# Kernel tuning notes

Measured on AMD Instinct MI355X. Metric: run time of the kernel, lower is better.

Reference implementation:

```python
import jax, jax.numpy as jnp
import numpy as np

K = 256       # num states
M = 2         # markov order
D = 256       # lemb_size
V = 50000     # ntypes (vocab)
T = 512
B = 256
Kp1 = K + 1
EPS = 1e-5
INIT = 0.1


def _layernorm(h, g, b):
    mu = h.mean(-1, keepdims=True)
    var = ((h - mu) ** 2).mean(-1, keepdims=True)
    return (h - mu) / jnp.sqrt(var + EPS) * g + b


def setup_inputs() -> dict:
    key = jax.random.key(0)
    ks = jax.random.split(key, 12)
    u = lambda k, shp: jax.random.uniform(k, shp, jnp.float32, -INIT, INIT)
    return {
        "x": jax.random.randint(ks[0], (T, B), 0, V, dtype=jnp.int32),
        "z": jax.random.randint(ks[1], (T, B), 0, K, dtype=jnp.int32),
        "lembs": u(ks[2], (K, D)),
        "tlembs": u(ks[3], (Kp1, D)),
        "dec_W": u(ks[4], (V, D)),
        "dec_b": jnp.zeros((V,), jnp.float32),
        "em_W": u(ks[5], (D, D)),
        "em_bias": jnp.zeros((D,), jnp.float32),
        "em_g": jnp.ones((D,), jnp.float32),
        "em_beta": jnp.zeros((D,), jnp.float32),
        "td_W": u(ks[6], (K, M * D)),
        "td_b": jnp.zeros((K,), jnp.float32),
        "tm_W": u(ks[7], (M * D, M * D)),
        "tm_bias": jnp.zeros((M * D,), jnp.float32),
        "tn_g": jnp.ones((M * D,), jnp.float32),
        "tn_beta": jnp.zeros((M * D,), jnp.float32),
    }


def reference(x, z, lembs, tlembs, dec_W, dec_b, em_W, em_bias, em_g, em_beta,
              td_W, td_b, tm_W, tm_bias, tn_g, tn_beta):
    # --- emission distribution: K x V log-normalized ---
    h = _layernorm(lembs + jax.nn.relu(lembs @ em_W.T + em_bias), em_g, em_beta)
    emdist = jax.nn.log_softmax(h @ dec_W.T + dec_b, axis=1)  # (K, V)

    # --- transition distribution: (Kp1^M, K) log-normalized ---
    # cartesian product of label embeddings, row-major: row r <-> (i_0,...,i_{M-1})
    idx = jnp.indices((Kp1,) * M).reshape(M, -1)                 # (M, Kp1^M)
    cat = tlembs[idx].transpose(1, 0, 2).reshape(-1, M * D)      # (Kp1^M, M*D)
    th = _layernorm(cat + jax.nn.relu(cat @ tm_W.T + tm_bias), tn_g, tn_beta)
    transdist = jax.nn.log_softmax(th @ td_W.T + td_b, axis=1)   # (Kp1^M, K)

    # --- log_joint ---
    xlps = emdist.T[x]                                           # (T, B, K)
    emlps = jnp.take_along_axis(xlps, z[..., None].astype(jnp.int32), axis=2)[..., 0].sum(0)  # (B,)

    zpad = jnp.concatenate([jnp.full((M, B), K, dtype=z.dtype), z], axis=0)  # (T+M, B)
    win = jnp.stack([zpad[m:m + T] for m in range(M + 1)], 0)    # (M+1, T, B)
    lin = win[0]
    for m in range(1, M):
        lin = lin * Kp1 + win[m]                                 # row index into (Kp1^M, K)
    trans_lps = transdist[lin, win[M]]                           # (T, B)
    return emlps + trans_lps.sum(0)                              # (B,)
```

## Files before the change

### kernel.cpp

```cpp
#include <hip/hip_runtime.h>

#define Kst 256
#define Dd 256
#define Vv 50000
#define VPAD 50176
#define Tt 512
#define Bb 256
#define KP1 257
#define MD 512
#define NROWS (KP1*KP1)
#define EPSf 1e-5f

#define VB2 196
#define VB3 (VB2*4)
#define EMB 800

typedef __attribute__((ext_vector_type(8))) short short8;
typedef __attribute__((ext_vector_type(4))) float f32x4;
typedef __attribute__((ext_vector_type(4))) unsigned u32x4;
typedef __attribute__((ext_vector_type(2))) unsigned u32x2;

__device__ __forceinline__ unsigned short f2bf(float f) {
    unsigned u = __builtin_bit_cast(unsigned, f);
    unsigned r = (u + 0x7fffu + ((u >> 16) & 1u)) >> 16;
    return (unsigned short)r;
}
__device__ __forceinline__ float bf2f(unsigned short u) {
    return __builtin_bit_cast(float, ((unsigned)u) << 16);
}
__device__ __forceinline__ unsigned bfpack(float lo, float hi) {
    return __builtin_amdgcn_perm(__builtin_bit_cast(unsigned, hi),
                                 __builtin_bit_cast(unsigned, lo), 0x07060302u);
}
__device__ __forceinline__ unsigned f2bf2(float lo, float hi) {
    return (unsigned)f2bf(lo) | ((unsigned)f2bf(hi) << 16);
}

__global__ __launch_bounds__(256) void k_hP(
    const float* __restrict__ lembs, const float* __restrict__ em_W,
    const float* __restrict__ em_bias, const float* __restrict__ em_g,
    const float* __restrict__ em_beta, unsigned short* __restrict__ h_bf,
    const float* __restrict__ tlembs, const float* __restrict__ tm_W,
    float* __restrict__ P0, float* __restrict__ P1,
    const float* __restrict__ td_W, const float* __restrict__ tn_g,
    const float* __restrict__ tn_beta, const float* __restrict__ td_b,
    unsigned short* __restrict__ tdwg_bf, float* __restrict__ Gt,
    float* __restrict__ Bt, const float* __restrict__ dec_W,
    unsigned short* __restrict__ dwP)
{
    int bid = blockIdx.x;
    int tid = threadIdx.x, lane = tid & 63, wv = tid >> 6;
    int l15 = lane & 15, q = lane >> 4;

    if (bid >= 108) {
        int pb = bid - 108;
        int vb2 = pb >> 1, sub = pb & 1;
        #pragma unroll 2
        for (int j = 0; j < 8; ++j) {
            int E0 = sub*4096 + wv*1024 + j*128 + lane*2;
            #pragma unroll
            for (int b = 0; b < 2; ++b) {
                int E = E0 + b;
                int ks = E >> 10, fi = (E >> 6) & 15, le = E & 63;
                int q2 = le >> 4, lv = le & 15;
                int v = ((fi >> 2) << 6) + lv*4 + (fi & 3);
                int row = vb2*256 + v;
                if (row > Vv-1) row = Vv-1;
                const float* src = dec_W + (size_t)row*Dd + ks*32 + q2*8;
                float4 f0 = *(const float4*)(src);
                float4 f1 = *(const float4*)(src + 4);
                u32x4 pk;
                pk.x = bfpack(f0.x, f0.y);
                pk.y = bfpack(f0.z, f0.w);
                pk.z = bfpack(f1.x, f1.y);
                pk.w = bfpack(f1.z, f1.w);
                *(short8*)(dwP + ((size_t)vb2*8192 + E)*8) = __builtin_bit_cast(short8, pk);
            }
        }
        return;
    }

    if (bid >= 44) {
        int c = (bid - 44)*4 + wv;
        const float4* w4 = (const float4*)(td_W + (size_t)c*MD);
        const float4* g4 = (const float4*)tn_g;
        const float4* b4 = (const float4*)tn_beta;
        float sg = 0.f, sb = 0.f;
        short8 o;
        #pragma unroll
        for (int u = 0; u < 2; ++u) {
            int j4 = lane*2 + u;
            float4 w = w4[j4], g = g4[j4], bt = b4[j4];
            sg += w.x*g.x + w.y*g.y + w.z*g.z + w.w*g.w;
            sb += w.x*bt.x + w.y*bt.y + w.z*bt.z + w.w*bt.w;
            o[u*4+0] = (short)f2bf(w.x*g.x);
            o[u*4+1] = (short)f2bf(w.y*g.y);
            o[u*4+2] = (short)f2bf(w.z*g.z);
            o[u*4+3] = (short)f2bf(w.w*g.w);
        }
        {
            int wvv = c >> 6, l15v = (c >> 2) & 15, ctv = c & 3;
            int ksv = lane >> 2, qv = lane & 3;
            *(short8*)(tdwg_bf +
                ((((size_t)wvv*16 + ksv)*4 + ctv)*64 + (qv*16 + l15v))*8) = o;
        }
        #pragma unroll
        for (int dd = 32; dd > 0; dd >>= 1) {
            sg += __shfl_xor(sg, dd);
            sb += __shfl_xor(sb, dd);
        }
        if (lane == 0) { Gt[c] = sg; Bt[c] = sb + td_b[c]; }
        return;
    }

    __shared__ short ta[32][264];
    __shared__ float lsep[4][32][2];
    __shared__ float musig[32][2];

    int job, r0, cb, koff, BK;
    const float* Arow; const float* Brow;
    if (bid < 8) {
        job = 0; r0 = bid*32; cb = 0; koff = 0; BK = Dd;
        Arow = lembs; Brow = em_W;
    } else {
        int b2 = bid - 8;
        int half = b2 / 18;
        int b3 = b2 % 18;
        job = 1 + half;
        r0 = (b3 >> 1) * 32;
        cb = (b3 & 1) * 256;
        koff = half * 256; BK = MD;
        Arow = tlembs; Brow = tm_W;
    }

    {
        int row = tid >> 3, seg = (tid & 7) * 32;
        int r = r0 + row;
        if (r > 256) r = 256;
        const float4* s4 = (const float4*)(Arow + (size_t)r*Dd + seg);
        #pragma unroll
        for (int u = 0; u < 4; ++u) {
            float4 f0 = s4[u*2], f1 = s4[u*2+1];
            u32x4 pk;
            pk.x = bfpack(f0.x, f0.y);
            pk.y = bfpack(f0.z, f0.w);
            pk.z = bfpack(f1.x, f1.y);
            pk.w = bfpack(f1.z, f1.w);
            *(short8*)&ta[row][seg + u*8] = __builtin_bit_cast(short8, pk);
        }
    }
    __syncthreads();

    const float* bptr[4];
    #pragma unroll
    for (int ct = 0; ct < 4; ++ct) {
        int j = cb + wv*64 + ct*16 + l15;
        bptr[ct] = Brow + (size_t)j*BK + koff + q*8;
    }
    f32x4 acc[2][4];
    #pragma unroll
    for (int rt = 0; rt < 2; ++rt)
        #pragma unroll
        for (int ct = 0; ct < 4; ++ct)
            acc[rt][ct] = (f32x4){0.f,0.f,0.f,0.f};
    for (int ks = 0; ks < 8; ++ks) {
        short8 a0 = *(const short8*)&ta[ 0 + l15][ks*32 + q*8];
        short8 a1 = *(const short8*)&ta[16 + l15][ks*32 + q*8];
        short8 b[4];
        #pragma unroll
        for (int ct = 0; ct < 4; ++ct) {
            float4 f0 = *(const float4*)(bptr[ct] + ks*32);
            float4 f1 = *(const float4*)(bptr[ct] + ks*32 + 4);
            u32x4 pk;
            pk.x = bfpack(f0.x, f0.y);
            pk.y = bfpack(f0.z, f0.w);
            pk.z = bfpack(f1.x, f1.y);
            pk.w = bfpack(f1.z, f1.w);
            b[ct] = __builtin_bit_cast(short8, pk);
        }
        #pragma unroll
        for (int ct = 0; ct < 4; ++ct) {
            acc[0][ct] = __builtin_amdgcn_mfma_f32_16x16x32_bf16(a0, b[ct], acc[0][ct], 0,0,0);
            acc[1][ct] = __builtin_amdgcn_mfma_f32_16x16x32_bf16(a1, b[ct], acc[1][ct], 0,0,0);
        }
    }

    if (job != 0) {
        float* Pd = (job == 1) ? P0 : P1;
        #pragma unroll
        for (int rt = 0; rt < 2; ++rt) {
            #pragma unroll
            for (int reg = 0; reg < 4; ++reg) {
                int r = r0 + rt*16 + q*4 + reg;
                if (r < KP1) {
                    float* dst = Pd + (size_t)r*MD + cb + wv*64;
                    #pragma unroll
                    for (int ct = 0; ct < 4; ++ct)
                        dst[ct*16 + l15] = acc[rt][ct][reg];
                }
            }
        }
        return;
    }

    float bias_c[4];
    #pragma unroll
    for (int ct = 0; ct < 4; ++ct)
        bias_c[ct] = em_bias[wv*64 + ct*16 + l15];
    #pragma unroll
    for (int rt = 0; rt < 2; ++rt) {
        #pragma unroll
        for (int reg = 0; reg < 4; ++reg) {
            int r = r0 + rt*16 + q*4 + reg;
            #pragma unroll
            for (int ct = 0; ct < 4; ++ct) {
                float lv = lembs[(size_t)r*Dd + wv*64 + ct*16 + l15];
                acc[rt][ct][reg] = lv + fmaxf(acc[rt][ct][reg] + bias_c[ct], 0.f);
            }
        }
    }
    #pragma unroll
    for (int rt = 0; rt < 2; ++rt) {
        #pragma unroll
        for (int reg = 0; reg < 4; ++reg) {
            float s  = ((acc[rt][0][reg] + acc[rt][1][reg]) + (acc[rt][2][reg] + acc[rt][3][reg]));
            float ss = ((acc[rt][0][reg]*acc[rt][0][reg] + acc[rt][1][reg]*acc[rt][1][reg])
                      + (acc[rt][2][reg]*acc[rt][2][reg] + acc[rt][3][reg]*acc[rt][3][reg]));
            s  += __shfl_xor(s, 1);  ss += __shfl_xor(ss, 1);
            s  += __shfl_xor(s, 2);  ss += __shfl_xor(ss, 2);
            s  += __shfl_xor(s, 4);  ss += __shfl_xor(ss, 4);
            s  += __shfl_xor(s, 8);  ss += __shfl_xor(ss, 8);
            if (l15 == 0) {
                int rw = rt*16 + q*4 + reg;
                lsep[wv][rw][0] = s;
                lsep[wv][rw][1] = ss;
            }
        }
    }
    __syncthreads();
    if (tid < 32) {
        float s  = (lsep[0][tid][0] + lsep[1][tid][0]) + (lsep[2][tid][0] + lsep[3][tid][0]);
        float ss = (lsep[0][tid][1] + lsep[1][tid][1]) + (lsep[2][tid][1] + lsep[3][tid][1]);
        float mu = s * (1.f/Dd);
        musig[tid][0] = mu;
        musig[tid][1] = rsqrtf(ss*(1.f/Dd) - mu*mu + EPSf);
    }
    __syncthreads();
    float gl[4], bl[4];
    #pragma unroll
    for (int ct = 0; ct < 4; ++ct) {
        gl[ct] = em_g[wv*64 + ct*16 + l15];
        bl[ct] = em_beta[wv*64 + ct*16 + l15];
    }
    #pragma unroll
    for (int rt = 0; rt < 2; ++rt) {
        #pragma unroll
        for (int reg = 0; reg < 4; ++reg) {
            int rw = rt*16 + q*4 + reg;
            int r = r0 + rw;
            float mu = musig[rw][0], rs = musig[rw][1];
            unsigned short* dst = h_bf + (size_t)r*Dd + wv*64;
            #pragma unroll
            for (int ct = 0; ct < 4; ++ct)
                dst[ct*16 + l15] = f2bf((acc[rt][ct][reg] - mu)*rs*gl[ct] + bl[ct]);
        }
    }
}

union SMemU {
    struct { short hs[64][264]; } em;
    struct { short th[32][520]; float musig[32][2]; float lsep[4][32][2]; } tr;
};

__global__ __launch_bounds__(256, 4) void k_emtrans(
    const unsigned short* __restrict__ dwP, const float* __restrict__ dec_b,
    const unsigned short* __restrict__ h_bf, float* __restrict__ part,
    unsigned short* __restrict__ E2,
    const float* __restrict__ tlembs, const float* __restrict__ P0,
    const float* __restrict__ P1, const float* __restrict__ tm_bias,
    const short* __restrict__ tdwg_bf, const float* __restrict__ Gt,
    const float* __restrict__ Bt, float* __restrict__ lse_t,
    unsigned short* __restrict__ Td)
{
    __shared__ SMemU sm;
    int bid = blockIdx.x;
    int tid = threadIdx.x, lane = tid & 63, wv = tid >> 6;
    int l15 = lane & 15, q = lane >> 4;

    if (bid < EMB) {
        int xcd = bid & 7, slot = bid >> 3;
        int grp = slot >> 2, kg = slot & 3;
        int vb = grp*8 + xcd;
        if (vb >= VB2) return;
        short (*hs)[264] = sm.em.hs;

        {
            int row = tid >> 2, c0 = (tid & 3) * 64;
            const short8* src = (const short8*)(h_bf + (size_t)(kg*64 + row)*Dd + c0);
            #pragma unroll
            for (int u = 0; u < 8; ++u)
                *(short8*)&hs[row][c0 + u*8] = src[u];
        }
        __syncthreads();

        f32x4 acc[4][4];
        #pragma unroll
        for (int mt = 0; mt < 4; ++mt)
            #pragma unroll
            for (int ct = 0; ct < 4; ++ct)
                acc[mt][ct] = (f32x4){0.f,0.f,0.f,0.f};

        const short8* bb8 = (const short8*)dwP + ((size_t)vb*8*16 + wv*4)*64 + lane;
        short8 Bf[3][4];
        #define LDB_EM(slot_, kk) { \
            Bf[slot_][0] = bb8[((kk)*16 + 0)*64]; \
            Bf[slot_][1] = bb8[((kk)*16 + 1)*64]; \
            Bf[slot_][2] = bb8[((kk)*16 + 2)*64]; \
            Bf[slot_][3] = bb8[((kk)*16 + 3)*64]; }
        LDB_EM(0, 0)
        LDB_EM(1, 1)
        #pragma unroll
        for (int ks = 0; ks < 8; ++ks) {
            if (ks < 6) LDB_EM((ks+2)%3, ks+2)
            short8 a[4];
            #pragma unroll
            for (int mt = 0; mt < 4; ++mt)
                a[mt] = *(const short8*)&hs[mt*16 + l15][ks*32 + q*8];
            #pragma unroll
            for (int mt = 0; mt < 4; ++mt)
                #pragma unroll
                for (int ct = 0; ct < 4; ++ct)
                    acc[mt][ct] = __builtin_amdgcn_mfma_f32_16x16x32_bf16(a[mt], Bf[ks%3][ct], acc[mt][ct], 0,0,0);
        }
        #undef LDB_EM

        int vcol[4]; bool vok[4];
        #pragma unroll
        for (int ct = 0; ct < 4; ++ct) {
            int v = vb*256 + wv*64 + l15*4 + ct;
            vok[ct] = (v < Vv);
            vcol[ct] = v < Vv ? v : Vv-1;
        }
        #pragma unroll
        for (int ct = 0; ct < 4; ++ct) {
            if (vok[ct]) {
                float db = dec_b[vcol[ct]];
                #pragma unroll
                for (int mt = 0; mt < 4; ++mt)
                    #pragma unroll
                    for (int reg = 0; reg < 4; ++reg)
                        acc[mt][ct][reg] += db;
            } else {
                #pragma unroll
                for (int mt = 0; mt < 4; ++mt)
                    #pragma unroll
                    for (int reg = 0; reg < 4; ++reg)
                        acc[mt][ct][reg] = -1e30f;
            }
        }
        #pragma unroll
        for (int mt = 0; mt < 4; ++mt) {
            #pragma unroll
            for (int reg = 0; reg < 4; ++reg) {
                int k = kg*64 + mt*16 + q*4 + reg;
                u32x2 p;
                p.x = f2bf2(acc[mt][0][reg], acc[mt][1][reg]);
                p.y = f2bf2(acc[mt][2][reg], acc[mt][3][reg]);
                *(u32x2*)(E2 + (size_t)k*VPAD + vb*256 + wv*64 + l15*4) = p;
            }
        }
        #pragma unroll
        for (int mt = 0; mt < 4; ++mt) {
            #pragma unroll
            for (int reg = 0; reg < 4; ++reg) {
                float m = fmaxf(fmaxf(acc[mt][0][reg], acc[mt][1][reg]),
                                fmaxf(acc[mt][2][reg], acc[mt][3][reg]));
                m = fmaxf(m, __shfl_xor(m, 1));
                m = fmaxf(m, __shfl_xor(m, 2));
                m = fmaxf(m, __shfl_xor(m, 4));
                m = fmaxf(m, __shfl_xor(m, 8));
                float s = __expf(acc[mt][0][reg] - m) + __expf(acc[mt][1][reg] - m)
                        + __expf(acc[mt][2][reg] - m) + __expf(acc[mt][3][reg] - m);
                s += __shfl_xor(s, 1);
                s += __shfl_xor(s, 2);
                s += __shfl_xor(s, 4);
                s += __shfl_xor(s, 8);
                if (l15 == 0) {
                    int k = kg*64 + mt*16 + q*4 + reg;
                    part[((size_t)k*VB3 + vb*4 + wv)*2]     = m;
                    part[((size_t)k*VB3 + vb*4 + wv)*2 + 1] = s;
                }
            }
        }
        return;
    }

    short (*th)[520]   = sm.tr.th;
    float (*musig)[2]  = sm.tr.musig;
    float (*lsep)[32][2] = sm.tr.lsep;
    int r0 = (bid - EMB) * 32;

    {
        const float4* bias0 = (const float4*)tm_bias;
        const float4* bias1 = (const float4*)(tm_bias + 256);
        float4 c0 = bias0[lane], c1 = bias1[lane];
        int i0a[8], i1a[8];
        #pragma unroll
        for (int i = 0; i < 8; ++i) {
            int r = r0 + wv*8 + i; if (r >= NROWS) r = NROWS - 1;
            i0a[i] = r / KP1; i1a[i] = r - i0a[i]*KP1;
        }
        #define ROWBODY(i, A0, B0, T0, A1, B1, T1) { \
            int row = wv*8 + (i); \
            float v0 = (T0).x + fmaxf((A0).x+(B0).x+c0.x, 0.f); \
            float v1 = (T0).y + fmaxf((A0).y+(B0).y+c0.y, 0.f); \
            float v2 = (T0).z + fmaxf((A0).z+(B0).z+c0.z, 0.f); \
            float v3 = (T0).w + fmaxf((A0).w+(B0).w+c0.w, 0.f); \
            float v4 = (T1).x + fmaxf((A1).x+(B1).x+c1.x, 0.f); \
            float v5 = (T1).y + fmaxf((A1).y+(B1).y+c1.y, 0.f); \
            float v6 = (T1).z + fmaxf((A1).z+(B1).z+c1.z, 0.f); \
            float v7 = (T1).w + fmaxf((A1).w+(B1).w+c1.w, 0.f); \
            u32x2 p0; p0.x = bfpack(v0, v1); p0.y = bfpack(v2, v3); \
            u32x2 p1; p1.x = bfpack(v4, v5); p1.y = bfpack(v6, v7); \
            *(u32x2*)&th[row][lane*4]       = p0; \
            *(u32x2*)&th[row][256 + lane*4] = p1; \
            float s  = ((v0+v1)+(v2+v3)) + ((v4+v5)+(v6+v7)); \
            float ss = ((v0*v0+v1*v1)+(v2*v2+v3*v3)) + ((v4*v4+v5*v5)+(v6*v6+v7*v7)); \
            _Pragma("unroll") \
            for (int d = 1; d < 64; d <<= 1) { \
                s  += __shfl_xor(s, d); \
                ss += __shfl_xor(ss, d); \
            } \
            if (lane == 0) { \
                float mu = s * (1.f/MD); \
                musig[row][0] = mu; \
                musig[row][1] = rsqrtf(ss*(1.f/MD) - mu*mu + EPSf); \
            } }

        if (i0a[0] == i0a[7]) {
            float4 A0 = ((const float4*)(P0 + (size_t)i0a[0]*MD))[lane];
            float4 A1 = ((const float4*)(P0 + (size_t)i0a[0]*MD + 256))[lane];
            float4 T0 = ((const float4*)(tlembs + (size_t)i0a[0]*Dd))[lane];
            #pragma unroll
            for (int i = 0; i < 8; ++i) {
                float4 b0 = ((const float4*)(P1 + (size_t)i1a[i]*MD))[lane];
                float4 b1 = ((const float4*)(P1 + (size_t)i1a[i]*MD + 256))[lane];
                float4 t1 = ((const float4*)(tlembs + (size_t)i1a[i]*Dd))[lane];
                ROWBODY(i, A0, b0, T0, A1, b1, t1)
            }
        } else {
            #pragma unroll
            for (int i = 0; i < 8; ++i) {
                float4 A0 = ((const float4*)(P0 + (size_t)i0a[i]*MD))[lane];
                float4 A1 = ((const float4*)(P0 + (size_t)i0a[i]*MD + 256))[lane];
                float4 T0 = ((const float4*)(tlembs + (size_t)i0a[i]*Dd))[lane];
                float4 b0 = ((const float4*)(P1 + (size_t)i1a[i]*MD))[lane];
                float4 b1 = ((const float4*)(P1 + (size_t)i1a[i]*MD + 256))[lane];
                float4 t1 = ((const float4*)(tlembs + (size_t)i1a[i]*Dd))[lane];
                ROWBODY(i, A0, b0, T0, A1, b1, t1)
            }
        }
        #undef ROWBODY
    }
    __syncthreads();

    f32x4 acc[2][4];
    #pragma unroll
    for (int rt = 0; rt < 2; ++rt)
        #pragma unroll
        for (int ct = 0; ct < 4; ++ct)
            acc[rt][ct] = (f32x4){0.f, 0.f, 0.f, 0.f};
    const short* bb = tdwg_bf + (size_t)wv*32768 + (size_t)lane*8;
    short8 Bf[3][4];
    #define LDB_TR(slot_, kk) { const short* nxt = bb + (size_t)(kk)*2048; \
        Bf[slot_][0] = *(const short8*)(nxt); \
        Bf[slot_][1] = *(const short8*)(nxt + 512); \
        Bf[slot_][2] = *(const short8*)(nxt + 1024); \
        Bf[slot_][3] = *(const short8*)(nxt + 1536); }
    LDB_TR(0, 0)
    LDB_TR(1, 1)
    #pragma unroll
    for (int ks = 0; ks < 16; ++ks) {
        if (ks < 14) LDB_TR((ks+2)%3, ks+2)
        int ko = ks*32 + q*8;
        short8 a0 = *(const short8*)&th[ 0 + l15][ko];
        short8 a1 = *(const short8*)&th[16 + l15][ko];
        acc[0][0] = __builtin_amdgcn_mfma_f32_16x16x32_bf16(a0, Bf[ks%3][0], acc[0][0], 0,0,0);
        acc[1][0] = __builtin_amdgcn_mfma_f32_16x16x32_bf16(a1, Bf[ks%3][0], acc[1][0], 0,0,0);
        acc[0][1] = __builtin_amdgcn_mfma_f32_16x16x32_bf16(a0, Bf[ks%3][1], acc[0][1], 0,0,0);
        acc[1][1] = __builtin_amdgcn_mfma_f32_16x16x32_bf16(a1, Bf[ks%3][1], acc[1][1], 0,0,0);
        acc[0][2] = __builtin_amdgcn_mfma_f32_16x16x32_bf16(a0, Bf[ks%3][2], acc[0][2], 0,0,0);
        acc[1][2] = __builtin_amdgcn_mfma_f32_16x16x32_bf16(a1, Bf[ks%3][2], acc[1][2], 0,0,0);
        acc[0][3] = __builtin_amdgcn_mfma_f32_16x16x32_bf16(a0, Bf[ks%3][3], acc[0][3], 0,0,0);
        acc[1][3] = __builtin_amdgcn_mfma_f32_16x16x32_bf16(a1, Bf[ks%3][3], acc[1][3], 0,0,0);
    }
    #undef LDB_TR

    float4 Gc = *(const float4*)(Gt + wv*64 + l15*4);
    float4 Bc = *(const float4*)(Bt + wv*64 + l15*4);
    #pragma unroll
    for (int rt = 0; rt < 2; ++rt) {
        #pragma unroll
        for (int reg = 0; reg < 4; ++reg) {
            int rw = rt*16 + q*4 + reg;
            float mu = musig[rw][0], rs = musig[rw][1];
            float e0 = rs*(acc[rt][0][reg] - mu*Gc.x) + Bc.x;
            float e1 = rs*(acc[rt][1][reg] - mu*Gc.y) + Bc.y;
            float e2 = rs*(acc[rt][2][reg] - mu*Gc.z) + Bc.z;
            float e3 = rs*(acc[rt][3][reg] - mu*Gc.w) + Bc.w;
            long r = (long)r0 + rw;
            if (r < NROWS) {
                u32x2 p;
                p.x = f2bf2(e0, e1);
                p.y = f2bf2(e2, e3);
                *(u32x2*)(Td + (size_t)r*Kst + wv*64 + l15*4) = p;
            }
            float m = fmaxf(fmaxf(e0, e1), fmaxf(e2, e3));
            m = fmaxf(m, __shfl_xor(m, 1));
            m = fmaxf(m, __shfl_xor(m, 2));
            m = fmaxf(m, __shfl_xor(m, 4));
            m = fmaxf(m, __shfl_xor(m, 8));
            float s = __expf(e0 - m) + __expf(e1 - m) + __expf(e2 - m) + __expf(e3 - m);
            s += __shfl_xor(s, 1);
            s += __shfl_xor(s, 2);
            s += __shfl_xor(s, 4);
            s += __shfl_xor(s, 8);
            if (l15 == 0) {
                lsep[wv][rw][0] = m;
                lsep[wv][rw][1] = s;
            }
        }
    }
    __syncthreads();
    if (tid < 32) {
        int r = r0 + tid;
        if (r < NROWS) {
            float m0 = lsep[0][tid][0], m1 = lsep[1][tid][0];
            float m2 = lsep[2][tid][0], m3 = lsep[3][tid][0];
            float mg = fmaxf(fmaxf(m0, m1), fmaxf(m2, m3));
            float s = lsep[0][tid][1]*__expf(m0-mg) + lsep[1][tid][1]*__expf(m1-mg)
                    + lsep[2][tid][1]*__expf(m2-mg) + lsep[3][tid][1]*__expf(m3-mg);
            lse_t[r] = mg + logf(s);
        }
    }
}

__global__ __launch_bounds__(64) void k_em_comb3(
    const float* __restrict__ part, float* __restrict__ lse_em)
{
    int k = blockIdx.x, lane = threadIdx.x;
    float m = -1e30f, s = 0.f;
    for (int vb = lane; vb < VB3; vb += 64) {
        float m2 = part[((size_t)k*VB3+vb)*2], s2 = part[((size_t)k*VB3+vb)*2+1];
        if (m2 > m) { s = s*__expf(m - m2) + s2; m = m2; }
        else          s += s2*__expf(m2 - m);
    }
    #pragma unroll
    for (int d = 1; d < 64; d <<= 1) {
        float mo = __shfl_xor(m, d), so = __shfl_xor(s, d);
        float mn = fmaxf(m, mo);
        s = s*__expf(m - mn) + so*__expf(mo - mn);
        m = mn;
    }
    if (lane == 0) lse_em[k] = m + logf(s);
}

#define GT_CH 2
__global__ __launch_bounds__(256) void k_gather3(
    const int* __restrict__ x, const int* __restrict__ z,
    const unsigned short* __restrict__ E2, const float* __restrict__ lse_em,
    const unsigned short* __restrict__ Td, const float* __restrict__ lse_t,
    float* __restrict__ out)
{
    int b = threadIdx.x;
    int t0 = blockIdx.x * GT_CH;
    float accv = 0.f;
    #pragma unroll
    for (int u = 0; u < GT_CH; ++u) {
        int t = t0 + u;
        int zc = z[t*Bb + b];
        int xv = x[t*Bb + b];
        int i0 = (t >= 2) ? z[(t-2)*Bb + b] : Kst;
        int i1 = (t >= 1) ? z[(t-1)*Bb + b] : Kst;
        int lin = i0*KP1 + i1;
        accv += bf2f(E2[(size_t)zc*VPAD + xv]) - lse_em[zc]
              + bf2f(Td[(size_t)lin*Kst + zc]) - lse_t[lin];
    }
    atomicAdd(&out[b], accv);
}

extern "C" void kernel_launch(void* const* d_in, const int* in_sizes, int n_in,
                              void* d_out, int out_size, void* d_ws, size_t ws_size,
                              hipStream_t stream)
{
    const int*   x       = (const int*)  d_in[0];
    const int*   z       = (const int*)  d_in[1];
    const float* lembs   = (const float*)d_in[2];
    const float* tlembs  = (const float*)d_in[3];
    const float* dec_W   = (const float*)d_in[4];
    const float* dec_b   = (const float*)d_in[5];
    const float* em_W    = (const float*)d_in[6];
    const float* em_bias = (const float*)d_in[7];
    const float* em_g    = (const float*)d_in[8];
    const float* em_beta = (const float*)d_in[9];
    const float* td_W    = (const float*)d_in[10];
    const float* td_b    = (const float*)d_in[11];
    const float* tm_W    = (const float*)d_in[12];
    const float* tm_bias = (const float*)d_in[13];
    const float* tn_g    = (const float*)d_in[14];
    const float* tn_beta = (const float*)d_in[15];
    float* out = (float*)d_out;

    float* ws     = (float*)d_ws;
    float* P0     = ws;
    float* P1     = P0 + 131584;
    float* lse_em = P1 + 131584;
    float* part   = lse_em + 256;
    float* lse_t  = part + 401408;
    float* Gt     = lse_t + 66052;
    float* Bt     = Gt + 256;
    unsigned short* tdwg_bf = (unsigned short*)(Bt + 256);
    unsigned short* h_bf   = tdwg_bf + 131072;
    unsigned short* E2     = h_bf + 65536;
    unsigned short* Td     = E2 + (size_t)Kst*VPAD;
    unsigned short* dwP    = Td + (size_t)NROWS*Kst;

    hipMemsetAsync(out, 0, Bb*sizeof(float), stream);
    k_hP<<<108 + 392, 256, 0, stream>>>(lembs, em_W, em_bias, em_g, em_beta, h_bf,
                                        tlembs, tm_W, P0, P1,
                                        td_W, tn_g, tn_beta, td_b, tdwg_bf, Gt, Bt,
                                        dec_W, dwP);
    k_emtrans<<<EMB + (NROWS + 31)/32, 256, 0, stream>>>(
        dwP, dec_b, h_bf, part, E2,
        tlembs, P0, P1, tm_bias, (const short*)tdwg_bf, Gt, Bt, lse_t, Td);
    k_em_comb3<<<Kst, 64, 0, stream>>>(part, lse_em);
    k_gather3<<<Tt/GT_CH, 256, 0, stream>>>(x, z, E2, lse_em, Td, lse_t, out);
}
```

Before: 204.4 us.

## Interleave emission and transition blocks, stage dec_W repack through LDS, add setprio

The fused emission/transition kernel now interleaves its work in groups of 56 blocks, 16 emission and 40 transition per group, instead of running all emission blocks first. The goal is to mix memory-heavy and MFMA-heavy blocks on each CU. The dec_W bf16 repack now uses one block per vocab tile and stages rows through LDS, so global reads are coalesced and writes go out in the packed layout. The MFMA loops are wrapped in s_setprio to favour matrix issue. The risks are tail imbalance from the new grid mapping and extra LDS synchronisation in the repack.

```diff
diff --git a/kernel.cpp b/kernel.cpp
--- a/kernel.cpp
+++ b/kernel.cpp
@@ -13,7 +13,11 @@
 
 #define VB2 196
 #define VB3 (VB2*4)
-#define EMB 800
+#define NTR ((NROWS+31)/32)
+#define GPER 56
+#define GEM  16
+#define NGRP 52
+#define GRID (GPER*NGRP)
 
 typedef __attribute__((ext_vector_type(8))) short short8;
 typedef __attribute__((ext_vector_type(4))) float f32x4;
@@ -35,6 +39,11 @@
 __device__ __forceinline__ unsigned f2bf2(float lo, float hi) {
     return (unsigned)f2bf(lo) | ((unsigned)f2bf(hi) << 16);
 }
+
+union HPU {
+    struct { short ta[32][264]; float lsep[4][32][2]; float musig[32][2]; } g;
+    struct { short pl[64][266]; } p;
+};
 
 __global__ __launch_bounds__(256) void k_hP(
     const float* __restrict__ lembs, const float* __restrict__ em_W,
@@ -48,33 +57,31 @@
     float* __restrict__ Bt, const float* __restrict__ dec_W,
     unsigned short* __restrict__ dwP)
 {
+    __shared__ HPU su;
     int bid = blockIdx.x;
     int tid = threadIdx.x, lane = tid & 63, wv = tid >> 6;
     int l15 = lane & 15, q = lane >> 4;
 
     if (bid >= 108) {
-        int pb = bid - 108;
-        int vb2 = pb >> 1, sub = pb & 1;
-        #pragma unroll 2
-        for (int j = 0; j < 8; ++j) {
-            int E0 = sub*4096 + wv*1024 + j*128 + lane*2;
-            #pragma unroll
-            for (int b = 0; b < 2; ++b) {
-                int E = E0 + b;
-                int ks = E >> 10, fi = (E >> 6) & 15, le = E & 63;
-                int q2 = le >> 4, lv = le & 15;
-                int v = ((fi >> 2) << 6) + lv*4 + (fi & 3);
-                int row = vb2*256 + v;
-                if (row > Vv-1) row = Vv-1;
-                const float* src = dec_W + (size_t)row*Dd + ks*32 + q2*8;
-                float4 f0 = *(const float4*)(src);
-                float4 f1 = *(const float4*)(src + 4);
-                u32x4 pk;
-                pk.x = bfpack(f0.x, f0.y);
-                pk.y = bfpack(f0.z, f0.w);
-                pk.z = bfpack(f1.x, f1.y);
-                pk.w = bfpack(f1.z, f1.w);
-                *(short8*)(dwP + ((size_t)vb2*8192 + E)*8) = __builtin_bit_cast(short8, pk);
+        int vb2 = bid - 108;
+        short (*pl)[266] = su.p.pl;
+        for (int c = 0; c < 4; ++c) {
+            if (c) __syncthreads();
+            int base_row = vb2*256 + c*64;
+            #pragma unroll 4
+            for (int i = 0; i < 16; ++i) {
+                int row = wv*16 + i;
+                int grow = base_row + row; if (grow > Vv-1) grow = Vv-1;
+                float4 f = ((const float4*)(dec_W + (size_t)grow*Dd))[lane];
+                u32x2 w; w.x = bfpack(f.x, f.y); w.y = bfpack(f.z, f.w);
+                *(u32x2*)&pl[row][lane*4] = w;
+            }
+            __syncthreads();
+            #pragma unroll
+            for (int i = 0; i < 8; ++i) {
+                short8 val = *(const short8*)&pl[(lane & 15)*4 + wv][i*32 + (lane >> 4)*8];
+                *(short8*)(dwP + ((size_t)vb2*8192 + (size_t)i*1024
+                                  + (c*4 + wv)*64 + lane)*8) = val;
             }
         }
         return;
@@ -113,9 +120,9 @@
         return;
     }
 
-    __shared__ short ta[32][264];
-    __shared__ float lsep[4][32][2];
-    __shared__ float musig[32][2];
+    short (*ta)[264] = su.g.ta;
+    float (*lsep)[32][2] = su.g.lsep;
+    float (*musig)[2] = su.g.musig;
 
     int job, r0, cb, koff, BK;
     const float* Arow; const float* Brow;
@@ -287,10 +294,12 @@
     int tid = threadIdx.x, lane = tid & 63, wv = tid >> 6;
     int l15 = lane & 15, q = lane >> 4;
 
-    if (bid < EMB) {
-        int xcd = bid & 7, slot = bid >> 3;
-        int grp = slot >> 2, kg = slot & 3;
-        int vb = grp*8 + xcd;
+    int grp = bid / GPER, rem = bid % GPER;
+    if (rem < GEM) {
+        int em_id = grp*GEM + rem;
+        int xcd = em_id & 7, slot = em_id >> 3;
+        int g2 = slot >> 2, kg = slot & 3;
+        int vb = g2*8 + xcd;
         if (vb >= VB2) return;
         short (*hs)[264] = sm.em.hs;
 
@@ -326,11 +335,13 @@
             #pragma unroll
             for (int mt = 0; mt < 4; ++mt)
                 a[mt] = *(const short8*)&hs[mt*16 + l15][ks*32 + q*8];
+            __builtin_amdgcn_s_setprio(1);
             #pragma unroll
             for (int mt = 0; mt < 4; ++mt)
                 #pragma unroll
                 for (int ct = 0; ct < 4; ++ct)
                     acc[mt][ct] = __builtin_amdgcn_mfma_f32_16x16x32_bf16(a[mt], Bf[ks%3][ct], acc[mt][ct], 0,0,0);
+            __builtin_amdgcn_s_setprio(0);
         }
         #undef LDB_EM
 
@@ -395,10 +406,12 @@
         return;
     }
 
+    int tr_id = grp*(GPER-GEM) + (rem - GEM);
+    if (tr_id >= NTR) return;
     short (*th)[520]   = sm.tr.th;
     float (*musig)[2]  = sm.tr.musig;
     float (*lsep)[32][2] = sm.tr.lsep;
-    int r0 = (bid - EMB) * 32;
+    int r0 = tr_id * 32;
 
     {
         const float4* bias0 = (const float4*)tm_bias;
@@ -485,6 +498,7 @@
         int ko = ks*32 + q*8;
         short8 a0 = *(const short8*)&th[ 0 + l15][ko];
         short8 a1 = *(const short8*)&th[16 + l15][ko];
+        __builtin_amdgcn_s_setprio(1);
         acc[0][0] = __builtin_amdgcn_mfma_f32_16x16x32_bf16(a0, Bf[ks%3][0], acc[0][0], 0,0,0);
         acc[1][0] = __builtin_amdgcn_mfma_f32_16x16x32_bf16(a1, Bf[ks%3][0], acc[1][0], 0,0,0);
         acc[0][1] = __builtin_amdgcn_mfma_f32_16x16x32_bf16(a0, Bf[ks%3][1], acc[0][1], 0,0,0);
@@ -493,6 +507,7 @@
         acc[1][2] = __builtin_amdgcn_mfma_f32_16x16x32_bf16(a1, Bf[ks%3][2], acc[1][2], 0,0,0);
         acc[0][3] = __builtin_amdgcn_mfma_f32_16x16x32_bf16(a0, Bf[ks%3][3], acc[0][3], 0,0,0);
         acc[1][3] = __builtin_amdgcn_mfma_f32_16x16x32_bf16(a1, Bf[ks%3][3], acc[1][3], 0,0,0);
+        __builtin_amdgcn_s_setprio(0);
     }
     #undef LDB_TR
 
@@ -626,11 +641,11 @@
     unsigned short* dwP    = Td + (size_t)NROWS*Kst;
 
     hipMemsetAsync(out, 0, Bb*sizeof(float), stream);
-    k_hP<<<108 + 392, 256, 0, stream>>>(lembs, em_W, em_bias, em_g, em_beta, h_bf,
+    k_hP<<<108 + VB2, 256, 0, stream>>>(lembs, em_W, em_bias, em_g, em_beta, h_bf,
                                         tlembs, tm_W, P0, P1,
                                         td_W, tn_g, tn_beta, td_b, tdwg_bf, Gt, Bt,
                                         dec_W, dwP);
-    k_emtrans<<<EMB + (NROWS + 31)/32, 256, 0, stream>>>(
+    k_emtrans<<<GRID, 256, 0, stream>>>(
         dwP, dec_b, h_bf, part, E2,
         tlembs, P0, P1, tm_bias, (const short*)tdwg_bf, Gt, Bt, lse_t, Td);
     k_em_comb3<<<Kst, 64, 0, stream>>>(part, lse_em);
```

Measured after the change: 213.1 us. 4.3% more time.
